# Performance work log

Hardware: AMD Instinct MI355X
Metric: run time of the kernel (lower is better)

Reference implementation:

```python
import jax, jax.numpy as jnp
import numpy as np

N = 100000
E = 1600000
IN_C = 128
OUT_C = 64
HID = 2 * OUT_C  # 128


def gcn_conv(x, src, dst, W, b, n):
    # PyG GCNConv with add_self_loops=True, symmetric normalization, bias.
    h = x @ W  # [n, d_out] - transform first (PyG order)
    ones = jnp.ones(src.shape[0], dtype=h.dtype)
    deg = jax.ops.segment_sum(ones, dst, num_segments=n)  # includes self-loops -> deg >= 1
    dinv = jax.lax.rsqrt(deg)
    norm = dinv[src] * dinv[dst]  # [E+n]
    msg = h[src] * norm[:, None]  # gather + scale
    return jax.ops.segment_sum(msg, dst, num_segments=n) + b


def setup_inputs() -> dict:
    key = jax.random.key(0)
    ks = jax.random.split(key, 8)
    x = jax.random.normal(ks[0], (N, IN_C), dtype=jnp.float32)
    edge_index = jax.random.randint(ks[1], (2, E), 0, N, dtype=jnp.int64)
    s1 = 1.0 / np.sqrt(IN_C)
    s2 = 1.0 / np.sqrt(HID)
    s3 = 1.0 / np.sqrt(OUT_C)
    W1 = jax.random.normal(ks[2], (IN_C, HID), dtype=jnp.float32) * s1
    b1 = jnp.zeros((HID,), dtype=jnp.float32)
    W2 = jax.random.normal(ks[3], (HID, OUT_C), dtype=jnp.float32) * s2
    b2 = jnp.zeros((OUT_C,), dtype=jnp.float32)
    Wfc = jax.random.normal(ks[4], (OUT_C, OUT_C), dtype=jnp.float32) * s3
    bfc = jax.random.uniform(ks[5], (OUT_C,), dtype=jnp.float32, minval=-s3, maxval=s3)
    return {"x": x, "edge_index": edge_index, "W1": W1, "b1": b1,
            "W2": W2, "b2": b2, "Wfc": Wfc, "bfc": bfc}


def reference(x, edge_index, W1, b1, W2, b2, Wfc, bfc):
    n = x.shape[0]
    loop = jnp.arange(n, dtype=edge_index.dtype)
    src = jnp.concatenate([edge_index[0], loop])  # add self-loops
    dst = jnp.concatenate([edge_index[1], loop])
    h = jax.nn.relu(gcn_conv(x, src, dst, W1, b1, n))
    h = gcn_conv(h, src, dst, W2, b2, n)
    return h @ Wfc + bfc
```

## Files before the change

### kernel.cpp

```cpp
#include <hip/hip_runtime.h>

#define INC  128
#define HIDC 128
#define OUTC 64

#define BSH   8
#define NBMAX 512
#define HB    128
#define TILE  4096
#define CAP   8192

typedef unsigned int  u32;
typedef unsigned short u16;
typedef short bf16x8 __attribute__((ext_vector_type(8)));
typedef float f32x4 __attribute__((ext_vector_type(4)));

static __device__ __forceinline__ u16 f2bf(float f) {
    u32 u = __builtin_bit_cast(u32, f);
    u += 0x7fffu + ((u >> 16) & 1u);
    return (u16)(u >> 16);
}
static __device__ __forceinline__ float bf_lo(u32 u) {
    return __builtin_bit_cast(float, u << 16);
}
static __device__ __forceinline__ float bf_hi(u32 u) {
    return __builtin_bit_cast(float, u & 0xffff0000u);
}


__global__ __launch_bounds__(256) void fold_bhist_kernel(const int* __restrict__ dst,
                                                         int* __restrict__ parts,
                                                         int E, int nb,
                                                         const float* __restrict__ W1,
                                                         const float* __restrict__ W2,
                                                         const float* __restrict__ Wfc,
                                                         const float* __restrict__ b2,
                                                         const float* __restrict__ bfc,
                                                         u16* __restrict__ W1t,
                                                         u16* __restrict__ W2ft,
                                                         float* __restrict__ b2f) {
    __shared__ int h[NBMAX];
    if (blockIdx.x < HB) {
        for (int i = threadIdx.x; i < NBMAX; i += 256) h[i] = 0;
        __syncthreads();
        const int total = HB * 256;
        for (int e = blockIdx.x * 256 + threadIdx.x; e < E; e += total)
            atomicAdd(&h[dst[e] >> BSH], 1);
        __syncthreads();
        for (int i = threadIdx.x; i < nb; i += 256) parts[i * HB + blockIdx.x] = h[i];
    } else {
        int t = (blockIdx.x - HB) * 256 + threadIdx.x;
        if (t < HIDC * HIDC) {
            int nn = t >> 7, k = t & 127;
            W1t[nn * HIDC + k] = f2bf(W1[k * HIDC + nn]);
        } else if (t < HIDC * HIDC + HIDC * OUTC) {
            int u = t - HIDC * HIDC;
            int i = u >> 6, j = u & 63;
            float s = 0.f;
#pragma unroll 8
            for (int k = 0; k < OUTC; ++k) s = fmaf(W2[i * OUTC + k], Wfc[k * OUTC + j], s);
            W2ft[j * HIDC + i] = f2bf(s);
        } else if (t < HIDC * HIDC + HIDC * OUTC + OUTC) {
            int j = t - HIDC * HIDC - HIDC * OUTC;
            float s = bfc[j];
#pragma unroll 8
            for (int k = 0; k < OUTC; ++k) s = fmaf(b2[k], Wfc[k * OUTC + j], s);
            b2f[j] = s;
        }
    }
}

__global__ __launch_bounds__(512) void bscan_kernel(const int* __restrict__ parts,
                                                    int* __restrict__ bucketOff, int nb) {
    __shared__ int sums[NBMAX];
    const int tid = threadIdx.x;
    int s = 0;
    if (tid < nb) {
        const int* p = parts + tid * HB;
#pragma unroll 8
        for (int r = 0; r < HB; ++r) s += p[r];
    }
    sums[tid] = s;
    __syncthreads();
    for (int d = 1; d < NBMAX; d <<= 1) {
        int t = sums[tid];
        int a = (tid >= d) ? sums[tid - d] : 0;
        __syncthreads();
        sums[tid] = t + a;
        __syncthreads();
    }
    if (tid < nb) bucketOff[tid] = sums[tid] - s;
    if (tid == NBMAX - 1) bucketOff[nb] = sums[NBMAX - 1];
}


template <int N, bool AF32, bool SCALED>
static __device__ __forceinline__ void gemm_body(char* smem, const void* __restrict__ Aptr,
                                                 const u16* __restrict__ Wt,
                                                 const float* __restrict__ dinv,
                                                 u16* __restrict__ out, int M, int bid) {
    constexpr int K = 128;
    constexpr int NC = N / 16;
    u16* Ws = (u16*)smem;

    const int tid = threadIdx.x;
    for (int id = tid; id < N * K / 8; id += 256) {
        int nn = id >> 4;
        int c  = id & 15;
        uint4 v = *(const uint4*)(Wt + nn * K + c * 8);
        int slot = (nn << 4) + (c ^ (nn & 7));
        *(uint4*)((char*)Ws + slot * 16) = v;
    }

    const int wave = tid >> 6;
    const int lane = tid & 63;
    const int r0   = bid * 64 + wave * 16;
    const int arow = r0 + (lane & 15);
    const int kgrp = lane >> 4;
    __syncthreads();

    f32x4 acc[NC];
#pragma unroll
    for (int nc = 0; nc < NC; ++nc) acc[nc] = f32x4{0.f, 0.f, 0.f, 0.f};

#pragma unroll
    for (int kc = 0; kc < 4; ++kc) {
        bf16x8 af = {0, 0, 0, 0, 0, 0, 0, 0};
        if (arow < M) {
            if constexpr (AF32) {
                const float* ap = (const float*)Aptr + (size_t)arow * K + kc * 32 + kgrp * 8;
                float4 v0 = *(const float4*)ap;
                float4 v1 = *(const float4*)(ap + 4);
                af[0] = (short)f2bf(v0.x); af[1] = (short)f2bf(v0.y);
                af[2] = (short)f2bf(v0.z); af[3] = (short)f2bf(v0.w);
                af[4] = (short)f2bf(v1.x); af[5] = (short)f2bf(v1.y);
                af[6] = (short)f2bf(v1.z); af[7] = (short)f2bf(v1.w);
            } else {
                af = *(const bf16x8*)((const u16*)Aptr + (size_t)arow * K + kc * 32 + kgrp * 8);
            }
        }
#pragma unroll
        for (int nc = 0; nc < NC; ++nc) {
            int nn = nc * 16 + (lane & 15);
            int slot = (nn << 4) + ((kc * 4 + kgrp) ^ (nn & 7));
            bf16x8 bfr = *(const bf16x8*)((const char*)Ws + slot * 16);
            acc[nc] = __builtin_amdgcn_mfma_f32_16x16x32_bf16(af, bfr, acc[nc], 0, 0, 0);
        }
    }
#pragma unroll
    for (int reg = 0; reg < 4; ++reg) {
        int row = r0 + (lane >> 4) * 4 + reg;
        if (row <= M) {
            float sc;
            if constexpr (SCALED) sc = (row < M) ? dinv[row] : 0.f;
            else                  sc = (row < M) ? 1.f : 0.f;
#pragma unroll
            for (int nc = 0; nc < NC; ++nc)
                out[(size_t)row * N + nc * 16 + (lane & 15)] = f2bf(acc[nc][reg] * sc);
        }
    }
}

static __device__ __forceinline__ void ms_body(char* smem,
                                               const int* __restrict__ src,
                                               const int* __restrict__ dst,
                                               const int* __restrict__ bucketOff,
                                               int* __restrict__ gfill,
                                               u32* __restrict__ binned,
                                               int E, int nb, int bid) {
    int2* buf   = (int2*)smem;
    int* hist   = (int*)(smem + TILE * 8);
    int* sbase  = hist + NBMAX;
    int* cursor = sbase + NBMAX;
    int* gposs  = cursor + NBMAX;
    int* wsum   = gposs + NBMAX;
    const int tid  = threadIdx.x;
    const int base = bid * TILE;
    const int cnt  = min(TILE, E - base);

    for (int i = tid; i < NBMAX; i += 256) hist[i] = 0;
    __syncthreads();

    int ls[16], ld[16], dg[16];
#pragma unroll
    for (int k = 0; k < 16; ++k) {
        int idx = tid + k * 256;
        if (idx < cnt) {
            ls[k] = src[base + idx];
            ld[k] = dst[base + idx];
            dg[k] = ld[k] >> BSH;
            atomicAdd(&hist[dg[k]], 1);
        } else dg[k] = -1;
    }
    __syncthreads();
    {
        const int a = hist[2 * tid], b = hist[2 * tid + 1];
        const int s = a + b;
        const int lane = tid & 63;
        int incl = s;
#pragma unroll
        for (int d = 1; d < 64; d <<= 1) {
            int t = __shfl_up(incl, d);
            if (lane >= d) incl += t;
        }
        if (lane == 63) wsum[tid >> 6] = incl;
        __syncthreads();
        const int w = tid >> 6;
        int wbase = 0;
        if (w > 0) wbase += wsum[0];
        if (w > 1) wbase += wsum[1];
        if (w > 2) wbase += wsum[2];
        const int excl = wbase + incl - s;
        sbase[2 * tid] = excl;          cursor[2 * tid] = excl;
        sbase[2 * tid + 1] = excl + a;  cursor[2 * tid + 1] = excl + a;
    }
    __syncthreads();
#pragma unroll
    for (int k = 0; k < 16; ++k) {
        if (dg[k] >= 0) {
            int p = atomicAdd(&cursor[dg[k]], 1);
            buf[p] = make_int2(ls[k], ld[k]);
        }
    }
    __syncthreads();
    for (int d = tid; d < nb; d += 256) {
        int c = cursor[d] - sbase[d];
        gposs[d] = (c > 0) ? atomicAdd(&gfill[d], c) : 0;
    }
    __syncthreads();
    for (int idx = tid; idx < cnt; idx += 256) {
        int2 e = buf[idx];
        int d = e.y >> BSH;
        binned[bucketOff[d] + gposs[d] + (idx - sbase[d])] =
            (u32)e.x | ((u32)(e.y & 255) << 24);
    }
}

#define SMEM_MERGED 41008

__global__ __launch_bounds__(256) void gemm1_ms_kernel(const float* __restrict__ x,
                                                       const u16* __restrict__ W1t,
                                                       u16* __restrict__ graw, int M,
                                                       const int* __restrict__ src,
                                                       const int* __restrict__ dst,
                                                       const int* __restrict__ bucketOff,
                                                       int* __restrict__ gfill,
                                                       u32* __restrict__ binned,
                                                       int E, int nb, int G) {
    __shared__ __align__(16) char smem[SMEM_MERGED];
    const int b = (int)blockIdx.x;
    if (b < G) gemm_body<HIDC, true, false>(smem, x, W1t, nullptr, graw, M, b);
    else       ms_body(smem, src, dst, bucketOff, gfill, binned, E, nb, b - G);
}

__global__ __launch_bounds__(256) void gemm2_kernel(const u16* __restrict__ h1,
                                                    const u16* __restrict__ W2ft,
                                                    const float* __restrict__ dinv,
                                                    u16* __restrict__ g2, int M) {
    __shared__ __align__(16) char smem[OUTC * 128 * 2];
    gemm_body<OUTC, false, true>(smem, h1, W2ft, dinv, g2, M, (int)blockIdx.x);
}


__global__ __launch_bounds__(256) void csr_build_kernel(const u32* __restrict__ binned,
                                                        const int* __restrict__ bucketOff,
                                                        int* __restrict__ col,
                                                        int* __restrict__ rowptr,
                                                        float* __restrict__ dinv,
                                                        int n, int E) {
    __shared__ int cnt[257];
    __shared__ int excl[256];
    __shared__ int wsum[4];
    __shared__ int colstage[CAP];
    const int tid   = threadIdx.x;
    const int b     = blockIdx.x;
    const int node0 = b << BSH;
    const int nNodes = min(256, n - node0);
    const int e0 = bucketOff[b], e1 = bucketOff[b + 1];
    const int ec = e1 - e0;

    for (int i = tid; i <= 256; i += 256) cnt[i] = 0;
    __syncthreads();
    for (int i = tid; i < ec; i += 256)
        atomicAdd(&cnt[binned[e0 + i] >> 24], 1);
    __syncthreads();
    const int myc = cnt[tid];
    {
        const int lane = tid & 63;
        int incl = myc;
#pragma unroll
        for (int d = 1; d < 64; d <<= 1) {
            int t = __shfl_up(incl, d);
            if (lane >= d) incl += t;
        }
        if (lane == 63) wsum[tid >> 6] = incl;
        __syncthreads();
        const int w = tid >> 6;
        int wbase = 0;
        if (w > 0) wbase += wsum[0];
        if (w > 1) wbase += wsum[1];
        if (w > 2) wbase += wsum[2];
        excl[tid] = wbase + incl - myc;
    }
    __syncthreads();
    if (tid < nNodes) {
        const int node = node0 + tid;
        rowptr[node] = e0 + excl[tid];
        dinv[node] = rsqrtf((float)(myc + 1));
    }
    if (b == 0 && tid == 0) { rowptr[n] = E; dinv[n] = 0.f; }
    __syncthreads();
    cnt[tid] = excl[tid];
    __syncthreads();
    if (ec <= CAP) {
        for (int i = tid; i < ec; i += 256) {
            u32 e = binned[e0 + i];
            int p = atomicAdd(&cnt[e >> 24], 1);
            colstage[p] = (int)(e & 0xffffffu);
        }
        __syncthreads();
        for (int i = tid; i < ec; i += 256) col[e0 + i] = colstage[i];
    } else {
        for (int i = tid; i < ec; i += 256) {
            u32 e = binned[e0 + i];
            int p = atomicAdd(&cnt[e >> 24], 1);
            col[e0 + p] = (int)(e & 0xffffffu);
        }
    }
}


__global__ __launch_bounds__(256) void agg1_kernel(const u16* __restrict__ g,
                                                   const int* __restrict__ rowptr,
                                                   const int* __restrict__ col,
                                                   const float* __restrict__ dinv,
                                                   const float* __restrict__ b1,
                                                   u32* __restrict__ h1, int n) {
    const int wid  = threadIdx.x >> 6;
    const int lane = threadIdx.x & 63;
    const int v = blockIdx.x * 4 + wid;
    if (v >= n) return;
    const int h = lane >> 5;
    const int r = lane & 31;
    const int base = rowptr[v], endi = rowptr[v + 1];
    const float dv = dinv[v];

    float a0 = 0.f, a1 = 0.f, a2 = 0.f, a3 = 0.f;
    float b0 = 0.f, b1v = 0.f, b2v = 0.f, b3 = 0.f;
    {
        uint2 sv = *(const uint2*)(g + ((size_t)v << 7) + (r << 2));
        if (h == 0) {
            a0 = dv * bf_lo(sv.x); a1 = dv * bf_hi(sv.x);
            a2 = dv * bf_lo(sv.y); a3 = dv * bf_hi(sv.y);
        }
    }

    for (int c = base; c < endi; c += 64) {
        const int m = min(64, endi - c);
        const int idx = (lane < m) ? col[c + lane] : n;
        const float wv = dinv[idx];
        for (int i = 0; i < m; i += 8) {
            int u0 = __shfl(idx, i + h);      float w0 = __shfl(wv, i + h);
            int u1 = __shfl(idx, i + 2 + h);  float w1 = __shfl(wv, i + 2 + h);
            int u2 = __shfl(idx, i + 4 + h);  float w2 = __shfl(wv, i + 4 + h);
            int u3 = __shfl(idx, i + 6 + h);  float w3 = __shfl(wv, i + 6 + h);
            uint2 x0 = *(const uint2*)(g + ((size_t)u0 << 7) + (r << 2));
            uint2 x1 = *(const uint2*)(g + ((size_t)u1 << 7) + (r << 2));
            uint2 x2 = *(const uint2*)(g + ((size_t)u2 << 7) + (r << 2));
            uint2 x3 = *(const uint2*)(g + ((size_t)u3 << 7) + (r << 2));
            a0 = fmaf(w0, bf_lo(x0.x), a0); a1 = fmaf(w0, bf_hi(x0.x), a1);
            a2 = fmaf(w0, bf_lo(x0.y), a2); a3 = fmaf(w0, bf_hi(x0.y), a3);
            b0 = fmaf(w1, bf_lo(x1.x), b0); b1v = fmaf(w1, bf_hi(x1.x), b1v);
            b2v = fmaf(w1, bf_lo(x1.y), b2v); b3 = fmaf(w1, bf_hi(x1.y), b3);
            a0 = fmaf(w2, bf_lo(x2.x), a0); a1 = fmaf(w2, bf_hi(x2.x), a1);
            a2 = fmaf(w2, bf_lo(x2.y), a2); a3 = fmaf(w2, bf_hi(x2.y), a3);
            b0 = fmaf(w3, bf_lo(x3.x), b0); b1v = fmaf(w3, bf_hi(x3.x), b1v);
            b2v = fmaf(w3, bf_lo(x3.y), b2v); b3 = fmaf(w3, bf_hi(x3.y), b3);
        }
    }
    float s0 = a0 + b0, s1 = a1 + b1v, s2 = a2 + b2v, s3 = a3 + b3;
    s0 += __shfl_xor(s0, 32);
    s1 += __shfl_xor(s1, 32);
    s2 += __shfl_xor(s2, 32);
    s3 += __shfl_xor(s3, 32);
    if (h == 0) {
        const float4 bb = *(const float4*)&b1[r << 2];
        float o0 = fmaxf(fmaf(dv, s0, bb.x), 0.f);
        float o1 = fmaxf(fmaf(dv, s1, bb.y), 0.f);
        float o2 = fmaxf(fmaf(dv, s2, bb.z), 0.f);
        float o3 = fmaxf(fmaf(dv, s3, bb.w), 0.f);
        uint2 pk;
        pk.x = (u32)f2bf(o0) | ((u32)f2bf(o1) << 16);
        pk.y = (u32)f2bf(o2) | ((u32)f2bf(o3) << 16);
        *(uint2*)(h1 + ((size_t)v << 6) + (r << 1)) = pk;
    }
}

__global__ __launch_bounds__(256) void agg2_kernel(const u16* __restrict__ g2,
                                                   const int* __restrict__ rowptr,
                                                   const int* __restrict__ col,
                                                   const float* __restrict__ dinv,
                                                   const float* __restrict__ b2f,
                                                   float* __restrict__ out, int n) {
    const int wid  = threadIdx.x >> 6;
    const int lane = threadIdx.x & 63;
    const int v = blockIdx.x * 4 + wid;
    if (v >= n) return;
    const int q = lane >> 4;
    const int r = lane & 15;
    const int base = rowptr[v], endi = rowptr[v + 1];

    float a0 = 0.f, a1 = 0.f, a2 = 0.f, a3 = 0.f;
    float b0 = 0.f, b1v = 0.f, b2v = 0.f, b3 = 0.f;
    {
        uint2 sv = *(const uint2*)(g2 + ((size_t)v << 6) + (r << 2));
        if (q == 0) {
            a0 = bf_lo(sv.x); a1 = bf_hi(sv.x);
            a2 = bf_lo(sv.y); a3 = bf_hi(sv.y);
        }
    }

    for (int c = base; c < endi; c += 64) {
        const int m = min(64, endi - c);
        const int idx = (lane < m) ? col[c + lane] : n;
        for (int i = 0; i < m; i += 8) {
            int u0 = __shfl(idx, i + q);
            int u1 = __shfl(idx, i + 4 + q);
            uint2 x0 = *(const uint2*)(g2 + ((size_t)u0 << 6) + (r << 2));
            uint2 x1 = *(const uint2*)(g2 + ((size_t)u1 << 6) + (r << 2));
            a0 += bf_lo(x0.x); a1 += bf_hi(x0.x); a2 += bf_lo(x0.y); a3 += bf_hi(x0.y);
            b0 += bf_lo(x1.x); b1v += bf_hi(x1.x); b2v += bf_lo(x1.y); b3 += bf_hi(x1.y);
        }
    }
    float s0 = a0 + b0, s1 = a1 + b1v, s2 = a2 + b2v, s3 = a3 + b3;
    s0 += __shfl_xor(s0, 16); s0 += __shfl_xor(s0, 32);
    s1 += __shfl_xor(s1, 16); s1 += __shfl_xor(s1, 32);
    s2 += __shfl_xor(s2, 16); s2 += __shfl_xor(s2, 32);
    s3 += __shfl_xor(s3, 16); s3 += __shfl_xor(s3, 32);
    if (q == 0) {
        const float dv = dinv[v];
        const float4 bb = *(const float4*)&b2f[r << 2];
        float4 o;
        o.x = fmaf(dv, s0, bb.x);
        o.y = fmaf(dv, s1, bb.y);
        o.z = fmaf(dv, s2, bb.z);
        o.w = fmaf(dv, s3, bb.w);
        *(float4*)(out + ((size_t)v << 6) + (r << 2)) = o;
    }
}


extern "C" void kernel_launch(void* const* d_in, const int* in_sizes, int n_in,
                              void* d_out, int out_size, void* d_ws, size_t ws_size,
                              hipStream_t stream) {
    const float* x   = (const float*)d_in[0];
    const int*   ei  = (const int*)d_in[1];
    const float* W1  = (const float*)d_in[2];
    const float* b1  = (const float*)d_in[3];
    const float* W2  = (const float*)d_in[4];
    const float* b2  = (const float*)d_in[5];
    const float* Wfc = (const float*)d_in[6];
    const float* bfc = (const float*)d_in[7];
    float* out = (float*)d_out;

    const int n = in_sizes[0] / INC;
    const int E = in_sizes[1] / 2;
    const int* src = ei;
    const int* dst = ei + E;
    const int nb = (n + 255) >> BSH;

    char* w = (char*)d_ws;
    auto alloc = [&](size_t bytes) -> void* {
        void* p = (void*)w;
        w += (bytes + 255) & ~(size_t)255;
        return p;
    };
    int*   rowptr    = (int*)alloc((size_t)(n + 1) * 4);
    float* dinvp     = (float*)alloc((size_t)(n + 1) * 4);
    int*   col       = (int*)alloc((size_t)(E + 64) * 4);
    u32*   binned    = (u32*)alloc((size_t)E * 4);
    int*   parts     = (int*)alloc((size_t)NBMAX * HB * 4);
    int*   bucketOff = (int*)alloc((size_t)(nb + 1) * 4);
    int*   gfill     = (int*)alloc((size_t)nb * 4);
    u16*   g         = (u16*)alloc((size_t)(n + 1) * HIDC * 2);
    u16*   h1        = (u16*)alloc((size_t)n * HIDC * 2);
    u16*   W1t       = (u16*)alloc((size_t)HIDC * HIDC * 2);
    u16*   W2ft      = (u16*)alloc((size_t)OUTC * HIDC * 2);
    float* b2f       = (float*)alloc((size_t)OUTC * 4);

    hipMemsetAsync(gfill, 0, (size_t)nb * 4, stream);

    const int FB = HB + (HIDC * HIDC + HIDC * OUTC + OUTC + 255) / 256;
    fold_bhist_kernel<<<FB, 256, 0, stream>>>(dst, parts, E, nb,
                                              W1, W2, Wfc, b2, bfc, W1t, W2ft, b2f);
    bscan_kernel<<<1, NBMAX, 0, stream>>>(parts, bucketOff, nb);

    const int G  = (n + 64) / 64;
    const int MS = (E + TILE - 1) / TILE;
    gemm1_ms_kernel<<<G + MS, 256, 0, stream>>>(x, W1t, g, n,
                                                src, dst, bucketOff, gfill, binned, E, nb, G);
    csr_build_kernel<<<nb, 256, 0, stream>>>(binned, bucketOff, col, rowptr, dinvp, n, E);

    agg1_kernel<<<(n + 3) / 4, 256, 0, stream>>>(g, rowptr, col, dinvp, b1, (u32*)h1, n);

    gemm2_kernel<<<(n + 64) / 64, 256, 0, stream>>>(h1, W2ft, dinvp, g, n);
    agg2_kernel<<<(n + 3) / 4, 256, 0, stream>>>(g, rowptr, col, dinvp, b2f, out, n);
}
```

Measured before the change: 190.2 us.

## Split agg1 feature dimension across two blocks with 4 neighbors per wave

The first-layer aggregation now splits each node's 128 features into two 64-feature halves, each handled by a separate block. Within a wave, four 16-lane groups gather four neighbors at once, using four independent accumulator sets and a two-step shuffle reduction. Blocks are interleaved so both halves of a node group are scheduled close together, to share L2 reuse of the column indices. The aim is more parallel waves and more memory-level parallelism per wave, at the cost of reading col and dinv twice and launching twice as many blocks.

```diff
diff --git a/kernel.cpp b/kernel.cpp
--- a/kernel.cpp
+++ b/kernel.cpp
@@ -336,20 +336,26 @@
                                                    const float* __restrict__ dinv,
                                                    const float* __restrict__ b1,
                                                    u32* __restrict__ h1, int n) {
+    const int bid  = (int)blockIdx.x;
+    const int half = (bid >> 2) & 1;
+    const int grp  = (bid >> 3) * 4 + (bid & 3);
     const int wid  = threadIdx.x >> 6;
     const int lane = threadIdx.x & 63;
-    const int v = blockIdx.x * 4 + wid;
+    const int v = grp * 4 + wid;
     if (v >= n) return;
-    const int h = lane >> 5;
-    const int r = lane & 31;
+    const int q = lane >> 4;
+    const int r = lane & 15;
     const int base = rowptr[v], endi = rowptr[v + 1];
     const float dv = dinv[v];
+    const size_t goff = ((size_t)half << 6) + (r << 2);
 
     float a0 = 0.f, a1 = 0.f, a2 = 0.f, a3 = 0.f;
     float b0 = 0.f, b1v = 0.f, b2v = 0.f, b3 = 0.f;
+    float c0 = 0.f, c1 = 0.f, c2 = 0.f, c3 = 0.f;
+    float d0 = 0.f, d1 = 0.f, d2 = 0.f, d3 = 0.f;
     {
-        uint2 sv = *(const uint2*)(g + ((size_t)v << 7) + (r << 2));
-        if (h == 0) {
+        uint2 sv = *(const uint2*)(g + ((size_t)v << 7) + goff);
+        if (q == 0) {
             a0 = dv * bf_lo(sv.x); a1 = dv * bf_hi(sv.x);
             a2 = dv * bf_lo(sv.y); a3 = dv * bf_hi(sv.y);
         }
@@ -359,32 +365,35 @@
         const int m = min(64, endi - c);
         const int idx = (lane < m) ? col[c + lane] : n;
         const float wv = dinv[idx];
-        for (int i = 0; i < m; i += 8) {
-            int u0 = __shfl(idx, i + h);      float w0 = __shfl(wv, i + h);
-            int u1 = __shfl(idx, i + 2 + h);  float w1 = __shfl(wv, i + 2 + h);
-            int u2 = __shfl(idx, i + 4 + h);  float w2 = __shfl(wv, i + 4 + h);
-            int u3 = __shfl(idx, i + 6 + h);  float w3 = __shfl(wv, i + 6 + h);
-            uint2 x0 = *(const uint2*)(g + ((size_t)u0 << 7) + (r << 2));
-            uint2 x1 = *(const uint2*)(g + ((size_t)u1 << 7) + (r << 2));
-            uint2 x2 = *(const uint2*)(g + ((size_t)u2 << 7) + (r << 2));
-            uint2 x3 = *(const uint2*)(g + ((size_t)u3 << 7) + (r << 2));
+        for (int i = 0; i < m; i += 16) {
+            int u0 = __shfl(idx, i + q);       float w0 = __shfl(wv, i + q);
+            int u1 = __shfl(idx, i + 4 + q);   float w1 = __shfl(wv, i + 4 + q);
+            int u2 = __shfl(idx, i + 8 + q);   float w2 = __shfl(wv, i + 8 + q);
+            int u3 = __shfl(idx, i + 12 + q);  float w3 = __shfl(wv, i + 12 + q);
+            uint2 x0 = *(const uint2*)(g + ((size_t)u0 << 7) + goff);
+            uint2 x1 = *(const uint2*)(g + ((size_t)u1 << 7) + goff);
+            uint2 x2 = *(const uint2*)(g + ((size_t)u2 << 7) + goff);
+            uint2 x3 = *(const uint2*)(g + ((size_t)u3 << 7) + goff);
             a0 = fmaf(w0, bf_lo(x0.x), a0); a1 = fmaf(w0, bf_hi(x0.x), a1);
             a2 = fmaf(w0, bf_lo(x0.y), a2); a3 = fmaf(w0, bf_hi(x0.y), a3);
             b0 = fmaf(w1, bf_lo(x1.x), b0); b1v = fmaf(w1, bf_hi(x1.x), b1v);
             b2v = fmaf(w1, bf_lo(x1.y), b2v); b3 = fmaf(w1, bf_hi(x1.y), b3);
-            a0 = fmaf(w2, bf_lo(x2.x), a0); a1 = fmaf(w2, bf_hi(x2.x), a1);
-            a2 = fmaf(w2, bf_lo(x2.y), a2); a3 = fmaf(w2, bf_hi(x2.y), a3);
-            b0 = fmaf(w3, bf_lo(x3.x), b0); b1v = fmaf(w3, bf_hi(x3.x), b1v);
-            b2v = fmaf(w3, bf_lo(x3.y), b2v); b3 = fmaf(w3, bf_hi(x3.y), b3);
-        }
-    }
-    float s0 = a0 + b0, s1 = a1 + b1v, s2 = a2 + b2v, s3 = a3 + b3;
-    s0 += __shfl_xor(s0, 32);
-    s1 += __shfl_xor(s1, 32);
-    s2 += __shfl_xor(s2, 32);
-    s3 += __shfl_xor(s3, 32);
-    if (h == 0) {
-        const float4 bb = *(const float4*)&b1[r << 2];
+            c0 = fmaf(w2, bf_lo(x2.x), c0); c1 = fmaf(w2, bf_hi(x2.x), c1);
+            c2 = fmaf(w2, bf_lo(x2.y), c2); c3 = fmaf(w2, bf_hi(x2.y), c3);
+            d0 = fmaf(w3, bf_lo(x3.x), d0); d1 = fmaf(w3, bf_hi(x3.x), d1);
+            d2 = fmaf(w3, bf_lo(x3.y), d2); d3 = fmaf(w3, bf_hi(x3.y), d3);
+        }
+    }
+    float s0 = (a0 + b0) + (c0 + d0);
+    float s1 = (a1 + b1v) + (c1 + d1);
+    float s2 = (a2 + b2v) + (c2 + d2);
+    float s3 = (a3 + b3) + (c3 + d3);
+    s0 += __shfl_xor(s0, 16); s0 += __shfl_xor(s0, 32);
+    s1 += __shfl_xor(s1, 16); s1 += __shfl_xor(s1, 32);
+    s2 += __shfl_xor(s2, 16); s2 += __shfl_xor(s2, 32);
+    s3 += __shfl_xor(s3, 16); s3 += __shfl_xor(s3, 32);
+    if (q == 0) {
+        const float4 bb = *(const float4*)&b1[(half << 6) + (r << 2)];
         float o0 = fmaxf(fmaf(dv, s0, bb.x), 0.f);
         float o1 = fmaxf(fmaf(dv, s1, bb.y), 0.f);
         float o2 = fmaxf(fmaf(dv, s2, bb.z), 0.f);
@@ -392,7 +401,7 @@
         uint2 pk;
         pk.x = (u32)f2bf(o0) | ((u32)f2bf(o1) << 16);
         pk.y = (u32)f2bf(o2) | ((u32)f2bf(o3) << 16);
-        *(uint2*)(h1 + ((size_t)v << 6) + (r << 1)) = pk;
+        *(uint2*)(h1 + ((size_t)v << 6) + (half << 5) + (r << 1)) = pk;
     }
 }
 
@@ -501,7 +510,8 @@
                                                 src, dst, bucketOff, gfill, binned, E, nb, G);
     csr_build_kernel<<<nb, 256, 0, stream>>>(binned, bucketOff, col, rowptr, dinvp, n, E);
 
-    agg1_kernel<<<(n + 3) / 4, 256, 0, stream>>>(g, rowptr, col, dinvp, b1, (u32*)h1, n);
+    const int ng = (n + 3) / 4;
+    agg1_kernel<<<8 * ((ng + 3) / 4), 256, 0, stream>>>(g, rowptr, col, dinvp, b1, (u32*)h1, n);
 
     gemm2_kernel<<<(n + 64) / 64, 256, 0, stream>>>(h1, W2ft, dinvp, g, n);
     agg2_kernel<<<(n + 3) / 4, 256, 0, stream>>>(g, rowptr, col, dinvp, b2f, out, n);
```

Result: slower. 207.8 us (+9.2%).
